# Optimization experiments

Measured on AMD Instinct MI355X. Metric: run time of the kernel, lower is better.

Reference implementation:

```python
import jax, jax.numpy as jnp
import numpy as np

N_PEP, N_MHC, N_TCR = 20000, 5000, 100000
EMB, HID = 128, 256
E_PM, E_MT = 200000, 400000
B = 50000


def setup_inputs() -> dict:
    key = jax.random.key(0)
    ks = jax.random.split(key, 30)
    f32 = jnp.float32

    def w(k, shape, fan_in):
        # torch Linear default: U(-1/sqrt(fan_in), 1/sqrt(fan_in))
        lim = 1.0 / np.sqrt(fan_in)
        return jax.random.uniform(k, shape, dtype=f32, minval=-lim, maxval=lim)

    inp = {
        # embedding tables (learned params)
        "emb_pep": jax.random.normal(ks[0], (N_PEP, EMB), dtype=f32),
        "emb_mhc": jax.random.normal(ks[1], (N_MHC, EMB), dtype=f32),
        "emb_tcr": jax.random.normal(ks[2], (N_TCR, EMB), dtype=f32),
        # edge lists (src=edge_index[0], dst=edge_index[1])
        "src_pm": jax.random.randint(ks[3], (E_PM,), 0, N_PEP, dtype=jnp.int32),
        "dst_pm": jax.random.randint(ks[4], (E_PM,), 0, N_MHC, dtype=jnp.int32),
        "src_mt": jax.random.randint(ks[5], (E_MT,), 0, N_MHC, dtype=jnp.int32),
        "dst_mt": jax.random.randint(ks[6], (E_MT,), 0, N_TCR, dtype=jnp.int32),
        # triplet pack indices
        "pack_pep": jax.random.randint(ks[7], (B,), 0, N_PEP, dtype=jnp.int32),
        "pack_mhc": jax.random.randint(ks[8], (B,), 0, N_MHC, dtype=jnp.int32),
        "pack_tcr": jax.random.randint(ks[9], (B,), 0, N_TCR, dtype=jnp.int32),
        # SAGEConv params: Wl (aggregated neighbors, with bias), Wr (root, no bias)
        # layer 1: pep->mhc (src 128, dst 128); mhc->tcr (src 128, dst 128)
        "l1_pm_Wl": w(ks[10], (HID, EMB), EMB), "l1_pm_bl": w(ks[11], (HID,), EMB),
        "l1_pm_Wr": w(ks[12], (HID, EMB), EMB),
        "l1_mt_Wl": w(ks[13], (HID, EMB), EMB), "l1_mt_bl": w(ks[14], (HID,), EMB),
        "l1_mt_Wr": w(ks[15], (HID, EMB), EMB),
        # layer 2: pep->mhc (src 128, dst 256); mhc->tcr (src 256, dst 256)
        "l2_pm_Wl": w(ks[16], (HID, EMB), EMB), "l2_pm_bl": w(ks[17], (HID,), EMB),
        "l2_pm_Wr": w(ks[18], (HID, HID), HID),
        "l2_mt_Wl": w(ks[19], (HID, HID), HID), "l2_mt_bl": w(ks[20], (HID,), HID),
        "l2_mt_Wr": w(ks[21], (HID, HID), HID),
        # proj_pep and head MLP
        "proj_W": w(ks[22], (HID, EMB), EMB), "proj_b": w(ks[23], (HID,), EMB),
        "head_W1": w(ks[24], (HID, 3 * HID), 3 * HID), "head_b1": w(ks[25], (HID,), 3 * HID),
        "head_W2": w(ks[26], (1, HID), HID), "head_b2": w(ks[27], (1,), HID),
    }
    return inp


def _sage(x_src, x_dst, src, dst, Wl, bl, Wr, n_dst):
    # SAGEConv(mean): lin_l(mean_{j in N(i)} x_src[j]) + lin_r(x_dst[i])
    msg = jax.ops.segment_sum(x_src[src], dst, num_segments=n_dst)  # [n_dst, d_src]
    cnt = jax.ops.segment_sum(jnp.ones((src.shape[0],), x_src.dtype), dst, num_segments=n_dst)
    mean = msg / jnp.maximum(cnt, 1.0)[:, None]
    return mean @ Wl.T + bl + x_dst @ Wr.T


def reference(emb_pep, emb_mhc, emb_tcr,
              src_pm, dst_pm, src_mt, dst_mt,
              pack_pep, pack_mhc, pack_tcr,
              l1_pm_Wl, l1_pm_bl, l1_pm_Wr, l1_mt_Wl, l1_mt_bl, l1_mt_Wr,
              l2_pm_Wl, l2_pm_bl, l2_pm_Wr, l2_mt_Wl, l2_mt_bl, l2_mt_Wr,
              proj_W, proj_b, head_W1, head_b1, head_W2, head_b2):
    relu = jax.nn.relu
    # layer 1 (HeteroConv reads all relations from the same input dict)
    mhc1 = relu(_sage(emb_pep, emb_mhc, src_pm, dst_pm, l1_pm_Wl, l1_pm_bl, l1_pm_Wr, N_MHC))
    tcr1 = relu(_sage(emb_mhc, emb_tcr, src_mt, dst_mt, l1_mt_Wl, l1_mt_bl, l1_mt_Wr, N_TCR))
    # layer 2 ('pep' is never a destination, so it keeps its embedding)
    mhc2 = relu(_sage(emb_pep, mhc1, src_pm, dst_pm, l2_pm_Wl, l2_pm_bl, l2_pm_Wr, N_MHC))
    tcr2 = relu(_sage(mhc1, tcr1, src_mt, dst_mt, l2_mt_Wl, l2_mt_bl, l2_mt_Wr, N_TCR))
    # projections + triplet gather (dropout disabled: inference)
    hp = (emb_pep @ proj_W.T + proj_b)[pack_pep]  # [B, HID]
    hm = mhc2[pack_mhc]
    ht = tcr2[pack_tcr]
    z = jnp.concatenate([hp, hm, ht], axis=-1)  # [B, 3*HID]
    hidden = relu(z @ head_W1.T + head_b1)
    logits = hidden @ head_W2.T + head_b2
    return logits.squeeze(-1)
```

## Files before the change

kernel.cpp:

```cpp
#include <hip/hip_runtime.h>

constexpr int NPEP = 20000, NMHC = 5000, NTCR = 100000;
constexpr int EPM = 200000, EMT = 400000, BB = 50000;
constexpr int MAXU = 50000;

typedef __attribute__((ext_vector_type(8))) short bf16x8;
typedef __attribute__((ext_vector_type(4))) float f32x4;

__device__ inline ushort f2bf(float x) {
    union { float f; unsigned u; } v; v.f = x;
    unsigned r = (v.u + 0x7FFF + ((v.u >> 16) & 1)) >> 16;
    return (ushort)r;
}
__device__ inline float bf2f(ushort b) {
    union { unsigned u; float f; } t; t.u = ((unsigned)b) << 16; return t.f;
}
__device__ inline void bf2x2(unsigned u, float& a, float& b) {
    union { unsigned x; float f; } t1, t2;
    t1.x = u << 16; t2.x = u & 0xffff0000u;
    a = t1.f; b = t2.f;
}
__device__ inline ushort4 f4bf(float4 v) {
    return make_ushort4(f2bf(v.x), f2bf(v.y), f2bf(v.z), f2bf(v.w));
}

__global__ __launch_bounds__(256) void prep_kernel(
    int* __restrict__ ibz,
    const float4* __restrict__ Wr1f, ushort4* __restrict__ Wr1_b,
    const float4* __restrict__ Wr2f, ushort4* __restrict__ Wr2_b,
    const float* __restrict__ head_W1, ushort4* __restrict__ W1b_b, ushort4* __restrict__ W1c_b,
    const float* __restrict__ l1_pm_Wl, const float* __restrict__ l1_pm_Wr,
    const float* __restrict__ l1_mt_Wl, ushort* __restrict__ Wcat1_b,
    const float* __restrict__ l2_pm_Wl, const float* __restrict__ l2_pm_Wr,
    const float* __restrict__ l2_mt_Wl, ushort* __restrict__ Wcat2_b,
    const float4* __restrict__ emb_mhc, ushort* __restrict__ Acat1,
    const float* __restrict__ proj_W, const float* __restrict__ proj_b,
    ushort* __restrict__ Wcomp_b, float* __restrict__ bp) {
    __shared__ float red[128];
    const int b = blockIdx.x, tid = threadIdx.x;
    if (b < 303) {
        int i = b * 256 + tid;
        if (i < 77500) ((int4*)ibz)[i] = make_int4(0, 0, 0, 0);
    } else if (b < 335) {
        int i = (b - 303) * 256 + tid;
        if (i < 8192) Wr1_b[i] = f4bf(Wr1f[i]);
    } else if (b < 399) {
        int i = (b - 335) * 256 + tid;
        if (i < 16384) Wr2_b[i] = f4bf(Wr2f[i]);
    } else if (b < 463) {
        int i = (b - 399) * 256 + tid;
        if (i < 16384) {
            int n = i >> 6, k4 = (i & 63) * 4;
            float4 v = *(const float4*)(head_W1 + (size_t)n * 768 + 256 + k4);
            W1b_b[i] = f4bf(v);
        }
    } else if (b < 527) {
        int i = (b - 463) * 256 + tid;
        if (i < 16384) {
            int n = i >> 6, k4 = (i & 63) * 4;
            float4 v = *(const float4*)(head_W1 + (size_t)n * 768 + 512 + k4);
            W1c_b[i] = f4bf(v);
        }
    } else if (b < 1039) {
        int idx = (b - 527) * 256 + tid;
        if (idx < 131072) {
            int r = idx >> 8, k = idx & 255;
            float v;
            if (r < 256) v = (k < 128) ? l1_pm_Wl[r * 128 + k] : l1_pm_Wr[r * 128 + (k - 128)];
            else         v = (k < 128) ? 0.f : l1_mt_Wl[(r - 256) * 128 + (k - 128)];
            Wcat1_b[idx] = f2bf(v);
        }
    } else if (b < 1807) {
        int idx = (b - 1039) * 256 + tid;
        if (idx < 196608) {
            int r = idx / 384, k = idx - r * 384;
            float v;
            if (r < 256) v = (k < 128) ? l2_pm_Wl[r * 128 + k] : l2_pm_Wr[r * 256 + (k - 128)];
            else         v = (k < 128) ? 0.f : l2_mt_Wl[(r - 256) * 256 + (k - 128)];
            Wcat2_b[idx] = f2bf(v);
        }
    } else if (b < 2432) {
        int i4 = (b - 1807) * 256 + tid;
        if (i4 < 160000) {
            int r = i4 >> 5, c4 = (i4 & 31) * 4;
            *(ushort4*)(Acat1 + (size_t)r * 256 + 128 + c4) = f4bf(emb_mhc[i4]);
        }
    } else {
        int i = b - 2432;
        const float* w1row = head_W1 + (size_t)i * 768;
        if (tid < 128) {
            float acc = 0.f;
            for (int k = 0; k < 256; k++) acc += w1row[k] * proj_W[k * 128 + tid];
            Wcomp_b[i * 128 + tid] = f2bf(acc);
            float pb = w1row[2 * tid] * proj_b[2 * tid] + w1row[2 * tid + 1] * proj_b[2 * tid + 1];
            red[tid] = pb;
        }
        __syncthreads();
        if (tid < 64) { red[tid] += red[tid + 64]; }
        __syncthreads();
        if (tid < 32) { red[tid] += red[tid + 32]; }
        __syncthreads();
        if (tid == 0) {
            float s = 0.f;
            for (int j = 0; j < 32; j++) s += red[j];
            bp[i] = s;
        }
    }
}

__global__ void hist2_kernel(const int* __restrict__ dst_pm, const int* __restrict__ dst_mt,
                             const int* __restrict__ pack_tcr,
                             int* __restrict__ deg_pm, int* __restrict__ deg_mt,
                             int* __restrict__ mark) {
    int t = blockIdx.x * blockDim.x + threadIdx.x;
    if (t < EPM) atomicAdd(&deg_pm[dst_pm[t]], 1);
    else if (t < EPM + EMT) atomicAdd(&deg_mt[dst_mt[t - EPM]], 1);
    else if (t < EPM + EMT + BB) mark[pack_tcr[t - EPM - EMT]] = 1;
}

__global__ __launch_bounds__(256) void blocksum2_kernel(const int* __restrict__ deg_pm,
                                                        const int* __restrict__ deg_mt,
                                                        const int* __restrict__ mark,
                                                        int* __restrict__ bsum_pm,
                                                        int* __restrict__ bsum_mt,
                                                        int* __restrict__ bsum_mk) {
    __shared__ int red[256];
    const int tid = threadIdx.x;
    const int* deg; int n, bi; int* bsum;
    if (blockIdx.x < 5) { deg = deg_pm; n = NMHC; bi = blockIdx.x; bsum = bsum_pm; }
    else if (blockIdx.x < 103) { deg = deg_mt; n = NTCR; bi = blockIdx.x - 5; bsum = bsum_mt; }
    else { deg = mark; n = NTCR; bi = blockIdx.x - 103; bsum = bsum_mk; }
    const int base = bi * 1024;
    int s = 0;
#pragma unroll
    for (int j = 0; j < 4; j++) {
        int i = base + tid + j * 256;
        if (i < n) s += deg[i];
    }
    red[tid] = s;
    __syncthreads();
    for (int off = 128; off > 0; off >>= 1) {
        if (tid < off) red[tid] += red[tid + off];
        __syncthreads();
    }
    if (tid == 0) bsum[bi] = red[0];
}

__global__ __launch_bounds__(128) void scanb2_kernel(int* __restrict__ bsum_pm,
                                                     int* __restrict__ bsum_mt,
                                                     int* __restrict__ bsum_mk) {
    __shared__ int s[128];
    const int tid = threadIdx.x;
    int* bsum = (blockIdx.x == 0) ? bsum_pm : ((blockIdx.x == 1) ? bsum_mt : bsum_mk);
    const int nb = (blockIdx.x == 0) ? 5 : 98;
    int v = (tid < nb) ? bsum[tid] : 0;
    s[tid] = v;
    __syncthreads();
    for (int off = 1; off < 128; off <<= 1) {
        int t = (tid >= off) ? s[tid - off] : 0;
        __syncthreads();
        s[tid] += t;
        __syncthreads();
    }
    if (tid < nb) bsum[tid] = (tid > 0) ? s[tid - 1] : 0;
    if (tid == 0) bsum[nb] = s[nb - 1];
}

__global__ __launch_bounds__(256) void emit2_kernel(const int* __restrict__ deg_pm,
                                                    const int* __restrict__ deg_mt,
                                                    const int* __restrict__ mark,
                                                    const int* __restrict__ bsum_pm,
                                                    const int* __restrict__ bsum_mt,
                                                    const int* __restrict__ bsum_mk,
                                                    int* __restrict__ rp_pm, float* __restrict__ cnt_pm,
                                                    int* __restrict__ rp_mt, float* __restrict__ cnt_mt,
                                                    int* __restrict__ list) {
    __shared__ int tsum[256];
    const int tid = threadIdx.x;
    const int* deg; const int* bsum; int* rp; float* cnt; int n, nb, bi, mode;
    if (blockIdx.x < 5) { deg = deg_pm; bsum = bsum_pm; rp = rp_pm; cnt = cnt_pm; n = NMHC; nb = 5; bi = blockIdx.x; mode = 0; }
    else if (blockIdx.x < 103) { deg = deg_mt; bsum = bsum_mt; rp = rp_mt; cnt = cnt_mt; n = NTCR; nb = 98; bi = blockIdx.x - 5; mode = 0; }
    else { deg = mark; bsum = bsum_mk; rp = nullptr; cnt = nullptr; n = NTCR; nb = 98; bi = blockIdx.x - 103; mode = 1; }
    const int i0 = bi * 1024 + tid * 4;
    int4 v = make_int4(0, 0, 0, 0);
    if (i0 + 3 < n) v = *(const int4*)(deg + i0);
    else if (i0 < n) {
        int t[4] = {0, 0, 0, 0};
        for (int j = 0; j < 4 && i0 + j < n; j++) t[j] = deg[i0 + j];
        v = make_int4(t[0], t[1], t[2], t[3]);
    }
    int s = v.x + v.y + v.z + v.w;
    tsum[tid] = s;
    __syncthreads();
    for (int off = 1; off < 256; off <<= 1) {
        int t = (tid >= off) ? tsum[tid - off] : 0;
        __syncthreads();
        tsum[tid] += t;
        __syncthreads();
    }
    int ex = ((tid > 0) ? tsum[tid - 1] : 0) + bsum[bi];
    if (mode == 0) {
        if (i0 + 3 < n) {
            int r1 = ex + v.x, r2 = r1 + v.y, r3 = r2 + v.z;
            *(int4*)(rp + i0) = make_int4(ex, r1, r2, r3);
            *(float4*)(cnt + i0) = make_float4((float)v.x, (float)v.y, (float)v.z, (float)v.w);
        } else if (i0 < n) {
            int r = ex;
            int vv[4] = {v.x, v.y, v.z, v.w};
            for (int j = 0; j < 4 && i0 + j < n; j++) {
                rp[i0 + j] = r;
                cnt[i0 + j] = (float)vv[j];
                r += vv[j];
            }
        }
        if (bi == 0 && tid == 0) rp[n] = bsum[nb];
    } else {
        int p = ex;
        int vv[4] = {v.x, v.y, v.z, v.w};
#pragma unroll
        for (int j = 0; j < 4; j++) {
            if (i0 + j < n && vv[j]) list[p++] = i0 + j;
        }
    }
}

__global__ void fill2_kernel(const int* __restrict__ src_pm, const int* __restrict__ dst_pm,
                             const int* __restrict__ src_mt, const int* __restrict__ dst_mt,
                             const int* __restrict__ rp_pm, int* __restrict__ cur_pm, int* __restrict__ csr_pm,
                             const int* __restrict__ rp_mt, int* __restrict__ cur_mt, int* __restrict__ csr_mt) {
    int t = blockIdx.x * blockDim.x + threadIdx.x;
    if (t < EPM) {
        int d = dst_pm[t];
        int pos = atomicAdd(&cur_pm[d], 1);
        csr_pm[rp_pm[d] + pos] = src_pm[t];
    } else if (t < EPM + EMT) {
        int t2 = t - EPM;
        int d = dst_mt[t2];
        int pos = atomicAdd(&cur_mt[d], 1);
        csr_mt[rp_mt[d] + pos] = src_mt[t2];
    }
}

__global__ __launch_bounds__(256) void gatherpm_kernel(const int* __restrict__ rp,
                                                       const int* __restrict__ csr_src,
                                                       const float* __restrict__ X,
                                                       ushort* __restrict__ A1, ushort* __restrict__ A2,
                                                       int n) {
    const int tid = threadIdx.x;
    const int r = blockIdx.x * 8 + (tid >> 5);
    const int lane = tid & 31;
    if (r >= n) return;
    const int e0 = rp[r], e1 = rp[r + 1];
    float4 s = make_float4(0.f, 0.f, 0.f, 0.f);
    for (int e = e0; e < e1; e++) {
        const int sidx = csr_src[e];
        float4 v = ((const float4*)(X + (long)sidx * 128))[lane];
        s.x += v.x; s.y += v.y; s.z += v.z; s.w += v.w;
    }
    float sc = 1.f / fmaxf((float)(e1 - e0), 1.f);
    ushort4 o = make_ushort4(f2bf(s.x * sc), f2bf(s.y * sc), f2bf(s.z * sc), f2bf(s.w * sc));
    *(ushort4*)(A1 + (size_t)r * 256 + lane * 4) = o;
    *(ushort4*)(A2 + (size_t)r * 384 + lane * 4) = o;
}

template <int K, int NB0, bool RELU0, bool G2>
__global__ __launch_bounds__(256, 2) void mfma_fused_kernel(
    int M, const ushort* __restrict__ A, const ushort* __restrict__ W,
    const float* __restrict__ bias,
    ushort* __restrict__ out0, int s0, ushort* __restrict__ out1) {
    constexpr int RS = 40;
    __shared__ ushort Als[128 * RS];
    __shared__ ushort Wls[128 * RS];
    const int tid = threadIdx.x;
    const int m0 = blockIdx.x * 128, n0 = blockIdx.y * 128;
    const int lane = tid & 63, w = tid >> 6;
    const int wm = w >> 1, wn = w & 1;
    const int m16 = lane & 15, q = lane >> 4;

    f32x4 acc[4][4] = {};

    for (int k0 = 0; k0 < K; k0 += 32) {
        bf16x8 a_st[2], w_st[2];
#pragma unroll
        for (int r = 0; r < 2; r++) {
            int chunk = tid + r * 256;
            int row = chunk >> 2, off = (chunk & 3) * 8;
            int ga = min(m0 + row, M - 1);
            a_st[r] = *(const bf16x8*)(A + (size_t)ga * K + k0 + off);
            w_st[r] = *(const bf16x8*)(W + (size_t)(n0 + row) * K + k0 + off);
        }
        __syncthreads();
#pragma unroll
        for (int r = 0; r < 2; r++) {
            int chunk = tid + r * 256;
            int row = chunk >> 2, off = (chunk & 3) * 8;
            *(bf16x8*)(&Als[row * RS + off]) = a_st[r];
            *(bf16x8*)(&Wls[row * RS + off]) = w_st[r];
        }
        __syncthreads();
        bf16x8 af[4], bf[4];
#pragma unroll
        for (int t = 0; t < 4; t++) {
            af[t] = *(const bf16x8*)(&Als[(wm * 64 + t * 16 + m16) * RS + q * 8]);
            bf[t] = *(const bf16x8*)(&Wls[(wn * 64 + t * 16 + m16) * RS + q * 8]);
        }
#pragma unroll
        for (int mt = 0; mt < 4; mt++)
#pragma unroll
            for (int nt = 0; nt < 4; nt++)
                acc[mt][nt] = __builtin_amdgcn_mfma_f32_16x16x32_bf16(af[mt], bf[nt], acc[mt][nt], 0, 0, 0);
    }

    const bool g1 = G2 && ((int)blockIdx.y >= NB0);
#pragma unroll
    for (int mt = 0; mt < 4; mt++) {
#pragma unroll
        for (int i = 0; i < 4; i++) {
            int row = m0 + wm * 64 + mt * 16 + q * 4 + i;
            if (row >= M) continue;
#pragma unroll
            for (int nt = 0; nt < 4; nt++) {
                int col = n0 + wn * 64 + nt * 16 + m16;
                float v = acc[mt][nt][i];
                if (!g1) {
                    v += bias[col];
                    if (RELU0) v = fmaxf(v, 0.f);
                    out0[(size_t)row * s0 + col] = f2bf(v);
                } else {
                    out1[(size_t)row * 256 + (col - NB0 * 128)] = f2bf(v);
                }
            }
        }
    }
}

__global__ __launch_bounds__(256, 3) void tcrall_kernel(
    const int* __restrict__ nrowsp, const int* __restrict__ list,
    const int* __restrict__ rp, const int* __restrict__ csr_src,
    const ushort* __restrict__ Z1, const ushort* __restrict__ Z2,
    const float* __restrict__ emb_tcr,
    const ushort* __restrict__ Wr1, const ushort* __restrict__ Wr2,
    const ushort* __restrict__ W1c,
    const float* __restrict__ bl1, const float* __restrict__ bl2,
    ushort* __restrict__ Ht) {
    constexpr int RS1 = 136;
    constexpr int RS2 = 264;
    __shared__ ushort B[32 * RS2];
    __shared__ ushort A1[32 * RS2];
    __shared__ ushort A2[32 * RS2];
    __shared__ int origs[32];
    const int tid = threadIdx.x;
    const int M = nrowsp[0];
    const int m0 = blockIdx.x * 32;
    if (m0 >= M) return;
    const int lane = tid & 63, w = tid >> 6;
    const int m16 = lane & 15, q = lane >> 4;

    if (tid < 32) origs[tid] = list[min(m0 + tid, M - 1)];

#pragma unroll
    for (int r = 0; r < 4; r++) {
        int chunk = tid + r * 256;
        int row = chunk >> 5, c4 = (chunk & 31) * 4;
        int grow = list[min(m0 + row, M - 1)];
        float4 v = *(const float4*)(emb_tcr + (size_t)grow * 128 + c4);
        *(ushort4*)(&B[row * RS1 + c4]) = f4bf(v);
    }

    {
        const int g = tid >> 5, gl = tid & 31;
        for (int rr = g; rr < 32; rr += 8) {
            int cr = min(m0 + rr, M - 1);
            int orig = list[cr];
            int e0 = rp[orig], e1 = rp[orig + 1];
            float s1[8] = {}, s2[8] = {};
            for (int e = e0; e < e1; e++) {
                int sidx = csr_src[e];
                uint4 u1 = *(const uint4*)(Z1 + (size_t)sidx * 256 + gl * 8);
                uint4 u2 = *(const uint4*)(Z2 + (size_t)sidx * 256 + gl * 8);
                float a, b;
                bf2x2(u1.x, a, b); s1[0] += a; s1[1] += b;
                bf2x2(u1.y, a, b); s1[2] += a; s1[3] += b;
                bf2x2(u1.z, a, b); s1[4] += a; s1[5] += b;
                bf2x2(u1.w, a, b); s1[6] += a; s1[7] += b;
                bf2x2(u2.x, a, b); s2[0] += a; s2[1] += b;
                bf2x2(u2.y, a, b); s2[2] += a; s2[3] += b;
                bf2x2(u2.z, a, b); s2[4] += a; s2[5] += b;
                bf2x2(u2.w, a, b); s2[6] += a; s2[7] += b;
            }
            float es = 1.f / fmaxf((float)(e1 - e0), 1.f);
            uint4 w1, w2;
            w1.x = (unsigned)f2bf(s1[0] * es) | ((unsigned)f2bf(s1[1] * es) << 16);
            w1.y = (unsigned)f2bf(s1[2] * es) | ((unsigned)f2bf(s1[3] * es) << 16);
            w1.z = (unsigned)f2bf(s1[4] * es) | ((unsigned)f2bf(s1[5] * es) << 16);
            w1.w = (unsigned)f2bf(s1[6] * es) | ((unsigned)f2bf(s1[7] * es) << 16);
            w2.x = (unsigned)f2bf(s2[0] * es) | ((unsigned)f2bf(s2[1] * es) << 16);
            w2.y = (unsigned)f2bf(s2[2] * es) | ((unsigned)f2bf(s2[3] * es) << 16);
            w2.z = (unsigned)f2bf(s2[4] * es) | ((unsigned)f2bf(s2[5] * es) << 16);
            w2.w = (unsigned)f2bf(s2[6] * es) | ((unsigned)f2bf(s2[7] * es) << 16);
            *(uint4*)(&A1[rr * RS2 + gl * 8]) = w1;
            *(uint4*)(&A2[rr * RS2 + gl * 8]) = w2;
        }
    }
    __syncthreads();

    {
        f32x4 acc[2][4] = {};
        for (int k0 = 0; k0 < 128; k0 += 32) {
            bf16x8 af[2], bf[4];
#pragma unroll
            for (int t = 0; t < 2; t++)
                af[t] = *(const bf16x8*)(&B[(t * 16 + m16) * RS1 + k0 + q * 8]);
#pragma unroll
            for (int t = 0; t < 4; t++)
                bf[t] = *(const bf16x8*)(Wr1 + (size_t)(w * 64 + t * 16 + m16) * 128 + k0 + q * 8);
#pragma unroll
            for (int mt = 0; mt < 2; mt++)
#pragma unroll
                for (int nt = 0; nt < 4; nt++)
                    acc[mt][nt] = __builtin_amdgcn_mfma_f32_16x16x32_bf16(af[mt], bf[nt], acc[mt][nt], 0, 0, 0);
        }
        __syncthreads();
#pragma unroll
        for (int mt = 0; mt < 2; mt++)
#pragma unroll
            for (int i = 0; i < 4; i++) {
                int lr = mt * 16 + q * 4 + i;
#pragma unroll
                for (int nt = 0; nt < 4; nt++) {
                    int col = w * 64 + nt * 16 + m16;
                    float v = acc[mt][nt][i] + bl1[col] + bf2f(A1[lr * RS2 + col]);
                    B[lr * RS2 + col] = f2bf(fmaxf(v, 0.f));
                }
            }
    }
    __syncthreads();

    {
        f32x4 acc[2][4] = {};
        for (int k0 = 0; k0 < 256; k0 += 32) {
            bf16x8 af[2], bf[4];
#pragma unroll
            for (int t = 0; t < 2; t++)
                af[t] = *(const bf16x8*)(&B[(t * 16 + m16) * RS2 + k0 + q * 8]);
#pragma unroll
            for (int t = 0; t < 4; t++)
                bf[t] = *(const bf16x8*)(Wr2 + (size_t)(w * 64 + t * 16 + m16) * 256 + k0 + q * 8);
#pragma unroll
            for (int mt = 0; mt < 2; mt++)
#pragma unroll
                for (int nt = 0; nt < 4; nt++)
                    acc[mt][nt] = __builtin_amdgcn_mfma_f32_16x16x32_bf16(af[mt], bf[nt], acc[mt][nt], 0, 0, 0);
        }
        __syncthreads();
#pragma unroll
        for (int mt = 0; mt < 2; mt++)
#pragma unroll
            for (int i = 0; i < 4; i++) {
                int lr = mt * 16 + q * 4 + i;
#pragma unroll
                for (int nt = 0; nt < 4; nt++) {
                    int col = w * 64 + nt * 16 + m16;
                    float v = acc[mt][nt][i] + bl2[col] + bf2f(A2[lr * RS2 + col]);
                    B[lr * RS2 + col] = f2bf(fmaxf(v, 0.f));
                }
            }
    }
    __syncthreads();

    {
        f32x4 acc[2][4] = {};
        for (int k0 = 0; k0 < 256; k0 += 32) {
            bf16x8 af[2], bf[4];
#pragma unroll
            for (int t = 0; t < 2; t++)
                af[t] = *(const bf16x8*)(&B[(t * 16 + m16) * RS2 + k0 + q * 8]);
#pragma unroll
            for (int t = 0; t < 4; t++)
                bf[t] = *(const bf16x8*)(W1c + (size_t)(w * 64 + t * 16 + m16) * 256 + k0 + q * 8);
#pragma unroll
            for (int mt = 0; mt < 2; mt++)
#pragma unroll
                for (int nt = 0; nt < 4; nt++)
                    acc[mt][nt] = __builtin_amdgcn_mfma_f32_16x16x32_bf16(af[mt], bf[nt], acc[mt][nt], 0, 0, 0);
        }
        __syncthreads();
#pragma unroll
        for (int mt = 0; mt < 2; mt++)
#pragma unroll
            for (int i = 0; i < 4; i++) {
                int lr = mt * 16 + q * 4 + i;
#pragma unroll
                for (int nt = 0; nt < 4; nt++) {
                    int col = w * 64 + nt * 16 + m16;
                    B[lr * RS2 + col] = f2bf(acc[mt][nt][i]);
                }
            }
    }
    __syncthreads();

#pragma unroll
    for (int r = 0; r < 4; r++) {
        int chunk = tid + r * 256;
        int row = chunk >> 5, c8 = (chunk & 31) * 8;
        if (m0 + row < M)
            *(uint4*)(Ht + (size_t)origs[row] * 256 + c8) = *(const uint4*)(&B[row * RS2 + c8]);
    }
}

template <int K, bool HASB, bool AF32>
__global__ __launch_bounds__(256, 2) void mfma_out_kernel(
    int M, const void* __restrict__ Av, const ushort* __restrict__ W,
    const float* __restrict__ bias, ushort* __restrict__ out) {
    constexpr int RS = 40;
    __shared__ ushort Als[128 * RS];
    __shared__ ushort Wls[128 * RS];
    const int tid = threadIdx.x;
    const int m0 = blockIdx.x * 128, n0 = blockIdx.y * 128;
    const int lane = tid & 63, w = tid >> 6;
    const int wm = w >> 1, wn = w & 1;
    const int m16 = lane & 15, q = lane >> 4;

    f32x4 acc[4][4] = {};

    for (int k0 = 0; k0 < K; k0 += 32) {
        bf16x8 a_st[2], w_st[2];
#pragma unroll
        for (int r = 0; r < 2; r++) {
            int chunk = tid + r * 256;
            int row = chunk >> 2, off = (chunk & 3) * 8;
            int ga = min(m0 + row, M - 1);
            if constexpr (AF32) {
                const float* Af = (const float*)Av;
                float4 f0 = *(const float4*)(Af + (size_t)ga * K + k0 + off);
                float4 f1 = *(const float4*)(Af + (size_t)ga * K + k0 + off + 4);
                ushort4 u0 = f4bf(f0), u1 = f4bf(f1);
                bf16x8 av;
                av[0] = (short)u0.x; av[1] = (short)u0.y; av[2] = (short)u0.z; av[3] = (short)u0.w;
                av[4] = (short)u1.x; av[5] = (short)u1.y; av[6] = (short)u1.z; av[7] = (short)u1.w;
                a_st[r] = av;
            } else {
                a_st[r] = *(const bf16x8*)((const ushort*)Av + (size_t)ga * K + k0 + off);
            }
            w_st[r] = *(const bf16x8*)(W + (size_t)(n0 + row) * K + k0 + off);
        }
        __syncthreads();
#pragma unroll
        for (int r = 0; r < 2; r++) {
            int chunk = tid + r * 256;
            int row = chunk >> 2, off = (chunk & 3) * 8;
            *(bf16x8*)(&Als[row * RS + off]) = a_st[r];
            *(bf16x8*)(&Wls[row * RS + off]) = w_st[r];
        }
        __syncthreads();
        bf16x8 af[4], bf[4];
#pragma unroll
        for (int t = 0; t < 4; t++) {
            af[t] = *(const bf16x8*)(&Als[(wm * 64 + t * 16 + m16) * RS + q * 8]);
            bf[t] = *(const bf16x8*)(&Wls[(wn * 64 + t * 16 + m16) * RS + q * 8]);
        }
#pragma unroll
        for (int mt = 0; mt < 4; mt++)
#pragma unroll
            for (int nt = 0; nt < 4; nt++)
                acc[mt][nt] = __builtin_amdgcn_mfma_f32_16x16x32_bf16(af[mt], bf[nt], acc[mt][nt], 0, 0, 0);
    }

#pragma unroll
    for (int mt = 0; mt < 4; mt++) {
#pragma unroll
        for (int i = 0; i < 4; i++) {
            int row = m0 + wm * 64 + mt * 16 + q * 4 + i;
            if (row >= M) continue;
#pragma unroll
            for (int nt = 0; nt < 4; nt++) {
                int col = n0 + wn * 64 + nt * 16 + m16;
                float v = acc[mt][nt][i];
                if (HASB) v += bias[col];
                out[(size_t)row * 256 + col] = f2bf(v);
            }
        }
    }
}

__global__ __launch_bounds__(256) void combine_kernel(
    const ushort* __restrict__ Hp, const ushort* __restrict__ Hm, const ushort* __restrict__ Ht,
    const int* __restrict__ pp, const int* __restrict__ pm, const int* __restrict__ pt,
    const float* __restrict__ b1, const float* __restrict__ W2, const float* __restrict__ b2,
    float* __restrict__ out) {
    const int tid = threadIdx.x;
    const int lane = tid & 63, w = tid >> 6;
    const int c = lane * 4;
    const float4 b1v = *(const float4*)(b1 + c);
    const float4 w2v = *(const float4*)(W2 + c);
    const float b2v = b2[0];
    const int base = blockIdx.x * 32 + w * 8;
#pragma unroll
    for (int t = 0; t < 8; t++) {
        int i = base + t;
        if (i >= BB) return;
        int ra = pp[i], rb = pm[i], rc = pt[i];
        ushort4 ua = *(const ushort4*)(Hp + (size_t)ra * 256 + c);
        ushort4 ub = *(const ushort4*)(Hm + (size_t)rb * 256 + c);
        ushort4 uc = *(const ushort4*)(Ht + (size_t)rc * 256 + c);
        float h0 = fmaxf(bf2f(ua.x) + bf2f(ub.x) + bf2f(uc.x) + b1v.x, 0.f);
        float h1 = fmaxf(bf2f(ua.y) + bf2f(ub.y) + bf2f(uc.y) + b1v.y, 0.f);
        float h2 = fmaxf(bf2f(ua.z) + bf2f(ub.z) + bf2f(uc.z) + b1v.z, 0.f);
        float h3 = fmaxf(bf2f(ua.w) + bf2f(ub.w) + bf2f(uc.w) + b1v.w, 0.f);
        float p = h0 * w2v.x + h1 * w2v.y + h2 * w2v.z + h3 * w2v.w;
#pragma unroll
        for (int off = 32; off > 0; off >>= 1) p += __shfl_down(p, off);
        if (lane == 0) out[i] = p + b2v;
    }
}

extern "C" void kernel_launch(void* const* d_in, const int* in_sizes, int n_in,
                              void* d_out, int out_size, void* d_ws, size_t ws_size,
                              hipStream_t stream) {
    const float* emb_pep = (const float*)d_in[0];
    const float* emb_mhc = (const float*)d_in[1];
    const float* emb_tcr = (const float*)d_in[2];
    const int* src_pm = (const int*)d_in[3];
    const int* dst_pm = (const int*)d_in[4];
    const int* src_mt = (const int*)d_in[5];
    const int* dst_mt = (const int*)d_in[6];
    const int* pack_pep = (const int*)d_in[7];
    const int* pack_mhc = (const int*)d_in[8];
    const int* pack_tcr = (const int*)d_in[9];
    const float* l1_pm_Wl = (const float*)d_in[10];
    const float* l1_pm_bl = (const float*)d_in[11];
    const float* l1_pm_Wr = (const float*)d_in[12];
    const float* l1_mt_Wl = (const float*)d_in[13];
    const float* l1_mt_bl = (const float*)d_in[14];
    const float* l1_mt_Wr = (const float*)d_in[15];
    const float* l2_pm_Wl = (const float*)d_in[16];
    const float* l2_pm_bl = (const float*)d_in[17];
    const float* l2_pm_Wr = (const float*)d_in[18];
    const float* l2_mt_Wl = (const float*)d_in[19];
    const float* l2_mt_bl = (const float*)d_in[20];
    const float* l2_mt_Wr = (const float*)d_in[21];
    const float* proj_W = (const float*)d_in[22];
    const float* proj_b = (const float*)d_in[23];
    const float* head_W1 = (const float*)d_in[24];
    const float* head_b1 = (const float*)d_in[25];
    const float* head_W2 = (const float*)d_in[26];
    const float* head_b2 = (const float*)d_in[27];
    float* out = (float*)d_out;

    int* ib = (int*)d_ws;
    int* deg_pm = ib;
    int* cur_pm = ib + 5000;
    int* deg_mt = ib + 10000;
    int* cur_mt = ib + 110000;
    int* mark   = ib + 210000;
    int* rp_pm  = ib + 310000;
    int* rp_mt  = ib + 315008;
    int* csr_pm = ib + 415016;
    int* csr_mt = ib + 615016;
    int* bsum_pm = ib + 1015016;
    int* bsum_mt = ib + 1015176;
    int* bsum_mk = ib + 1015336;
    int* list    = ib + 1015496;

    float* f = (float*)(ib + 1065544);
    float* cnt_pm = f;
    float* cnt_mt = f + 5000;
    float* bp     = f + 105000;

    ushort* u = (ushort*)(f + 105344);
    ushort* Wcat1_b = u;
    ushort* Wcat2_b = u + 131072;
    ushort* W1b_b   = u + 327680;
    ushort* W1c_b   = u + 393216;
    ushort* Wcomp_b = u + 458752;
    ushort* Wr1_b   = u + 491520;
    ushort* Wr2_b   = u + 524288;
    ushort* Acat1   = u + 589824;
    ushort* Acat2   = u + 1869824;
    ushort* Zb1     = u + 3789824;
    ushort* Zb2     = u + 5069824;
    ushort* mhc2_b  = u + 6349824;
    ushort* Hp_b    = u + 7629824;
    ushort* Hm_b    = u + 12749824;
    ushort* Ht_b    = u + 14029824;

    prep_kernel<<<2688, 256, 0, stream>>>(
        ib,
        (const float4*)l1_mt_Wr, (ushort4*)Wr1_b,
        (const float4*)l2_mt_Wr, (ushort4*)Wr2_b,
        head_W1, (ushort4*)W1b_b, (ushort4*)W1c_b,
        l1_pm_Wl, l1_pm_Wr, l1_mt_Wl, Wcat1_b,
        l2_pm_Wl, l2_pm_Wr, l2_mt_Wl, Wcat2_b,
        (const float4*)emb_mhc, Acat1,
        proj_W, proj_b, Wcomp_b, bp);

    hist2_kernel<<<(EPM + EMT + BB + 255) / 256, 256, 0, stream>>>(
        dst_pm, dst_mt, pack_tcr, deg_pm, deg_mt, mark);
    blocksum2_kernel<<<201, 256, 0, stream>>>(deg_pm, deg_mt, mark, bsum_pm, bsum_mt, bsum_mk);
    scanb2_kernel<<<3, 128, 0, stream>>>(bsum_pm, bsum_mt, bsum_mk);
    emit2_kernel<<<201, 256, 0, stream>>>(deg_pm, deg_mt, mark, bsum_pm, bsum_mt, bsum_mk,
                                          rp_pm, cnt_pm, rp_mt, cnt_mt, list);
    fill2_kernel<<<(EPM + EMT + 255) / 256, 256, 0, stream>>>(
        src_pm, dst_pm, src_mt, dst_mt, rp_pm, cur_pm, csr_pm, rp_mt, cur_mt, csr_mt);

    gatherpm_kernel<<<(NMHC + 7) / 8, 256, 0, stream>>>(rp_pm, csr_pm, emb_pep, Acat1, Acat2, NMHC);

    mfma_fused_kernel<256, 2, true, true><<<dim3((NMHC + 127) / 128, 4), 256, 0, stream>>>(
        NMHC, Acat1, Wcat1_b, l1_pm_bl, Acat2 + 128, 384, Zb1);
    mfma_fused_kernel<384, 2, true, true><<<dim3((NMHC + 127) / 128, 4), 256, 0, stream>>>(
        NMHC, Acat2, Wcat2_b, l2_pm_bl, mhc2_b, 256, Zb2);

    tcrall_kernel<<<(MAXU + 31) / 32, 256, 0, stream>>>(
        bsum_mk + 98, list, rp_mt, csr_mt, Zb1, Zb2, emb_tcr,
        Wr1_b, Wr2_b, W1c_b, l1_mt_bl, l2_mt_bl, Ht_b);

    mfma_out_kernel<128, true, true><<<dim3((NPEP + 127) / 128, 2), 256, 0, stream>>>(
        NPEP, emb_pep, Wcomp_b, bp, Hp_b);
    mfma_out_kernel<256, false, false><<<dim3((NMHC + 127) / 128, 2), 256, 0, stream>>>(
        NMHC, mhc2_b, W1b_b, nullptr, Hm_b);

    combine_kernel<<<(BB + 31) / 32, 256, 0, stream>>>(
        Hp_b, Hm_b, Ht_b, pack_pep, pack_mhc, pack_tcr,
        head_b1, head_W2, head_b2, out);
}
```

Measured before the change: 416.3 us.

## Merge output GEMMs into gather/tcr kernels and compact TCR output rows

Folds the two standalone output GEMM launches into existing kernels by block-range dispatch: the pep projection tile runs inside the MHC gather kernel, and the mhc2×W1b tile runs inside the TCR kernel using a shared-memory union. The TCR kernel now writes results to compacted rows, with an inverse map built during emit and a remapped pack_tcr index used by combine, so the scattered stores to a full 100k-row buffer go away. The neighbor loop preloads up to 32 CSR indices per lane and broadcasts them with shuffles, and the unused float degree-count writes are removed. This cuts launch count and scattered traffic, but adds an extra indirection buffer and gives the merged kernels uneven per-block work.

```diff
diff --git a/kernel.cpp b/kernel.cpp
--- a/kernel.cpp
+++ b/kernel.cpp
@@ -22,6 +22,81 @@
 }
 __device__ inline ushort4 f4bf(float4 v) {
     return make_ushort4(f2bf(v.x), f2bf(v.y), f2bf(v.z), f2bf(v.w));
+}
+
+constexpr int RS  = 40;
+constexpr int RS1 = 136;
+constexpr int RS2 = 264;
+
+template <int K, bool HASB, bool AF32>
+__device__ void out_tile(ushort* Als, ushort* Wls, int tid, int bx, int by, int M,
+                         const void* __restrict__ Av, const ushort* __restrict__ W,
+                         const float* __restrict__ bias, ushort* __restrict__ out) {
+    const int m0 = bx * 128, n0 = by * 128;
+    const int lane = tid & 63, w = tid >> 6;
+    const int wm = w >> 1, wn = w & 1;
+    const int m16 = lane & 15, q = lane >> 4;
+
+    f32x4 acc[4][4] = {};
+
+    for (int k0 = 0; k0 < K; k0 += 32) {
+        bf16x8 a_st[2], w_st[2];
+#pragma unroll
+        for (int r = 0; r < 2; r++) {
+            int chunk = tid + r * 256;
+            int row = chunk >> 2, off = (chunk & 3) * 8;
+            int ga = min(m0 + row, M - 1);
+            if constexpr (AF32) {
+                const float* Af = (const float*)Av;
+                float4 f0 = *(const float4*)(Af + (size_t)ga * K + k0 + off);
+                float4 f1 = *(const float4*)(Af + (size_t)ga * K + k0 + off + 4);
+                ushort4 u0 = f4bf(f0), u1 = f4bf(f1);
+                bf16x8 av;
+                av[0] = (short)u0.x; av[1] = (short)u0.y; av[2] = (short)u0.z; av[3] = (short)u0.w;
+                av[4] = (short)u1.x; av[5] = (short)u1.y; av[6] = (short)u1.z; av[7] = (short)u1.w;
+                a_st[r] = av;
+            } else {
+                a_st[r] = *(const bf16x8*)((const ushort*)Av + (size_t)ga * K + k0 + off);
+            }
+            w_st[r] = *(const bf16x8*)(W + (size_t)(n0 + row) * K + k0 + off);
+        }
+        __syncthreads();
+#pragma unroll
+        for (int r = 0; r < 2; r++) {
+            int chunk = tid + r * 256;
+            int row = chunk >> 2, off = (chunk & 3) * 8;
+            *(bf16x8*)(&Als[row * RS + off]) = a_st[r];
+            *(bf16x8*)(&Wls[row * RS + off]) = w_st[r];
+        }
+        __syncthreads();
+        bf16x8 af[4], bf[4];
+#pragma unroll
+        for (int t = 0; t < 4; t++) {
+            af[t] = *(const bf16x8*)(&Als[(wm * 64 + t * 16 + m16) * RS + q * 8]);
+            bf[t] = *(const bf16x8*)(&Wls[(wn * 64 + t * 16 + m16) * RS + q * 8]);
+        }
+#pragma unroll
+        for (int mt = 0; mt < 4; mt++)
+#pragma unroll
+            for (int nt = 0; nt < 4; nt++)
+                acc[mt][nt] = __builtin_amdgcn_mfma_f32_16x16x32_bf16(af[mt], bf[nt], acc[mt][nt], 0, 0, 0);
+    }
+
+#pragma unroll
+    for (int mt = 0; mt < 4; mt++) {
+#pragma unroll
+        for (int i = 0; i < 4; i++) {
+            int row = m0 + wm * 64 + mt * 16 + q * 4 + i;
+            if (row >= M) continue;
+#pragma unroll
+            for (int nt = 0; nt < 4; nt++) {
+                int col = n0 + wn * 64 + nt * 16 + m16;
+                float v = acc[mt][nt][i];
+                if (HASB) v += bias[col];
+                out[(size_t)row * 256 + col] = f2bf(v);
+            }
+        }
+    }
 }
 
 __global__ __launch_bounds__(256) void prep_kernel(
@@ -51,15 +126,13 @@
         int i = (b - 399) * 256 + tid;
         if (i < 16384) {
             int n = i >> 6, k4 = (i & 63) * 4;
-            float4 v = *(const float4*)(head_W1 + (size_t)n * 768 + 256 + k4);
-            W1b_b[i] = f4bf(v);
+            W1b_b[i] = f4bf(*(const float4*)(head_W1 + (size_t)n * 768 + 256 + k4));
         }
     } else if (b < 527) {
         int i = (b - 463) * 256 + tid;
         if (i < 16384) {
             int n = i >> 6, k4 = (i & 63) * 4;
-            float4 v = *(const float4*)(head_W1 + (size_t)n * 768 + 512 + k4);
-            W1c_b[i] = f4bf(v);
+            W1c_b[i] = f4bf(*(const float4*)(head_W1 + (size_t)n * 768 + 512 + k4));
         }
     } else if (b < 1039) {
         int idx = (b - 527) * 256 + tid;
@@ -92,8 +165,7 @@
             float acc = 0.f;
             for (int k = 0; k < 256; k++) acc += w1row[k] * proj_W[k * 128 + tid];
             Wcomp_b[i * 128 + tid] = f2bf(acc);
-            float pb = w1row[2 * tid] * proj_b[2 * tid] + w1row[2 * tid + 1] * proj_b[2 * tid + 1];
-            red[tid] = pb;
+            red[tid] = w1row[2 * tid] * proj_b[2 * tid] + w1row[2 * tid + 1] * proj_b[2 * tid + 1];
         }
         __syncthreads();
         if (tid < 64) { red[tid] += red[tid + 64]; }
@@ -172,15 +244,16 @@
                                                     const int* __restrict__ bsum_pm,
                                                     const int* __restrict__ bsum_mt,
                                                     const int* __restrict__ bsum_mk,
-                                                    int* __restrict__ rp_pm, float* __restrict__ cnt_pm,
-                                                    int* __restrict__ rp_mt, float* __restrict__ cnt_mt,
-                                                    int* __restrict__ list) {
+                                                    int* __restrict__ rp_pm,
+                                                    int* __restrict__ rp_mt,
+                                                    int* __restrict__ list,
+                                                    int* __restrict__ inv) {
     __shared__ int tsum[256];
     const int tid = threadIdx.x;
-    const int* deg; const int* bsum; int* rp; float* cnt; int n, nb, bi, mode;
-    if (blockIdx.x < 5) { deg = deg_pm; bsum = bsum_pm; rp = rp_pm; cnt = cnt_pm; n = NMHC; nb = 5; bi = blockIdx.x; mode = 0; }
-    else if (blockIdx.x < 103) { deg = deg_mt; bsum = bsum_mt; rp = rp_mt; cnt = cnt_mt; n = NTCR; nb = 98; bi = blockIdx.x - 5; mode = 0; }
-    else { deg = mark; bsum = bsum_mk; rp = nullptr; cnt = nullptr; n = NTCR; nb = 98; bi = blockIdx.x - 103; mode = 1; }
+    const int* deg; const int* bsum; int* rp; int n, nb, bi, mode;
+    if (blockIdx.x < 5) { deg = deg_pm; bsum = bsum_pm; rp = rp_pm; n = NMHC; nb = 5; bi = blockIdx.x; mode = 0; }
+    else if (blockIdx.x < 103) { deg = deg_mt; bsum = bsum_mt; rp = rp_mt; n = NTCR; nb = 98; bi = blockIdx.x - 5; mode = 0; }
+    else { deg = mark; bsum = bsum_mk; rp = nullptr; n = NTCR; nb = 98; bi = blockIdx.x - 103; mode = 1; }
     const int i0 = bi * 1024 + tid * 4;
     int4 v = make_int4(0, 0, 0, 0);
     if (i0 + 3 < n) v = *(const int4*)(deg + i0);
@@ -189,8 +262,7 @@
         for (int j = 0; j < 4 && i0 + j < n; j++) t[j] = deg[i0 + j];
         v = make_int4(t[0], t[1], t[2], t[3]);
     }
-    int s = v.x + v.y + v.z + v.w;
-    tsum[tid] = s;
+    tsum[tid] = v.x + v.y + v.z + v.w;
     __syncthreads();
     for (int off = 1; off < 256; off <<= 1) {
         int t = (tid >= off) ? tsum[tid - off] : 0;
@@ -203,15 +275,10 @@
         if (i0 + 3 < n) {
             int r1 = ex + v.x, r2 = r1 + v.y, r3 = r2 + v.z;
             *(int4*)(rp + i0) = make_int4(ex, r1, r2, r3);
-            *(float4*)(cnt + i0) = make_float4((float)v.x, (float)v.y, (float)v.z, (float)v.w);
         } else if (i0 < n) {
             int r = ex;
             int vv[4] = {v.x, v.y, v.z, v.w};
-            for (int j = 0; j < 4 && i0 + j < n; j++) {
-                rp[i0 + j] = r;
-                cnt[i0 + j] = (float)vv[j];
-                r += vv[j];
-            }
+            for (int j = 0; j < 4 && i0 + j < n; j++) { rp[i0 + j] = r; r += vv[j]; }
         }
         if (bi == 0 && tid == 0) rp[n] = bsum[nb];
     } else {
@@ -219,7 +286,7 @@
         int vv[4] = {v.x, v.y, v.z, v.w};
 #pragma unroll
         for (int j = 0; j < 4; j++) {
-            if (i0 + j < n && vv[j]) list[p++] = i0 + j;
+            if (i0 + j < n && vv[j]) { list[p] = i0 + j; inv[i0 + j] = p; p++; }
         }
     }
 }
@@ -241,26 +308,39 @@
     }
 }
 
-__global__ __launch_bounds__(256) void gatherpm_kernel(const int* __restrict__ rp,
-                                                       const int* __restrict__ csr_src,
-                                                       const float* __restrict__ X,
-                                                       ushort* __restrict__ A1, ushort* __restrict__ A2,
-                                                       int n) {
+__global__ __launch_bounds__(256, 2) void gph_kernel(
+    const int* __restrict__ rp, const int* __restrict__ csr_src,
+    const float* __restrict__ X, ushort* __restrict__ A1, ushort* __restrict__ A2,
+    const float* __restrict__ emb_pep, const ushort* __restrict__ Wcomp,
+    const float* __restrict__ bp, ushort* __restrict__ Hp,
+    const int* __restrict__ pack_tcr, const int* __restrict__ inv, int* __restrict__ pt_c) {
+    __shared__ ushort Als[128 * RS];
+    __shared__ ushort Wls[128 * RS];
     const int tid = threadIdx.x;
-    const int r = blockIdx.x * 8 + (tid >> 5);
-    const int lane = tid & 31;
-    if (r >= n) return;
-    const int e0 = rp[r], e1 = rp[r + 1];
-    float4 s = make_float4(0.f, 0.f, 0.f, 0.f);
-    for (int e = e0; e < e1; e++) {
-        const int sidx = csr_src[e];
-        float4 v = ((const float4*)(X + (long)sidx * 128))[lane];
-        s.x += v.x; s.y += v.y; s.z += v.z; s.w += v.w;
-    }
-    float sc = 1.f / fmaxf((float)(e1 - e0), 1.f);
-    ushort4 o = make_ushort4(f2bf(s.x * sc), f2bf(s.y * sc), f2bf(s.z * sc), f2bf(s.w * sc));
-    *(ushort4*)(A1 + (size_t)r * 256 + lane * 4) = o;
-    *(ushort4*)(A2 + (size_t)r * 384 + lane * 4) = o;
+    const int b = blockIdx.x;
+    if (b < 625) {
+        const int r = b * 8 + (tid >> 5);
+        const int lane = tid & 31;
+        if (r >= NMHC) return;
+        const int e0 = rp[r], e1 = rp[r + 1];
+        float4 s = make_float4(0.f, 0.f, 0.f, 0.f);
+        for (int e = e0; e < e1; e++) {
+            const int sidx = csr_src[e];
+            float4 v = ((const float4*)(X + (long)sidx * 128))[lane];
+            s.x += v.x; s.y += v.y; s.z += v.z; s.w += v.w;
+        }
+        float sc = 1.f / fmaxf((float)(e1 - e0), 1.f);
+        ushort4 o = make_ushort4(f2bf(s.x * sc), f2bf(s.y * sc), f2bf(s.z * sc), f2bf(s.w * sc));
+        *(ushort4*)(A1 + (size_t)r * 256 + lane * 4) = o;
+        *(ushort4*)(A2 + (size_t)r * 384 + lane * 4) = o;
+    } else if (b < 939) {
+        int v = b - 625;
+        out_tile<128, true, true>(Als, Wls, tid, v % 157, v / 157, NPEP,
+                                  emb_pep, Wcomp, bp, Hp);
+    } else {
+        int i = (b - 939) * 256 + tid;
+        if (i < BB) pt_c[i] = inv[pack_tcr[i]];
+    }
 }
 
 template <int K, int NB0, bool RELU0, bool G2>
@@ -268,7 +348,6 @@
     int M, const ushort* __restrict__ A, const ushort* __restrict__ W,
     const float* __restrict__ bias,
     ushort* __restrict__ out0, int s0, ushort* __restrict__ out1) {
-    constexpr int RS = 40;
     __shared__ ushort Als[128 * RS];
     __shared__ ushort Wls[128 * RS];
     const int tid = threadIdx.x;
@@ -334,7 +413,7 @@
     }
 }
 
-__global__ __launch_bounds__(256, 3) void tcrall_kernel(
+__global__ __launch_bounds__(256, 3) void tcrhm_kernel(
     const int* __restrict__ nrowsp, const int* __restrict__ list,
     const int* __restrict__ rp, const int* __restrict__ csr_src,
     const ushort* __restrict__ Z1, const ushort* __restrict__ Z2,
@@ -342,29 +421,36 @@
     const ushort* __restrict__ Wr1, const ushort* __restrict__ Wr2,
     const ushort* __restrict__ W1c,
     const float* __restrict__ bl1, const float* __restrict__ bl2,
-    ushort* __restrict__ Ht) {
-    constexpr int RS1 = 136;
-    constexpr int RS2 = 264;
-    __shared__ ushort B[32 * RS2];
-    __shared__ ushort A1[32 * RS2];
-    __shared__ ushort A2[32 * RS2];
-    __shared__ int origs[32];
+    ushort* __restrict__ Ht_c,
+    const ushort* __restrict__ mhc2, const ushort* __restrict__ W1b,
+    ushort* __restrict__ Hm) {
+    union SM {
+        struct { ushort B[32 * RS2]; ushort A1[32 * RS2]; ushort A2[32 * RS2]; } t;
+        struct { ushort Als[128 * RS]; ushort Wls[128 * RS]; } g;
+    };
+    __shared__ SM sm;
     const int tid = threadIdx.x;
+
+    if (blockIdx.x >= 1563) {
+        int v = blockIdx.x - 1563;
+        out_tile<256, false, false>(sm.g.Als, sm.g.Wls, tid, v % 40, v / 40, NMHC,
+                                    mhc2, W1b, nullptr, Hm);
+        return;
+    }
+
     const int M = nrowsp[0];
     const int m0 = blockIdx.x * 32;
     if (m0 >= M) return;
     const int lane = tid & 63, w = tid >> 6;
     const int m16 = lane & 15, q = lane >> 4;
 
-    if (tid < 32) origs[tid] = list[min(m0 + tid, M - 1)];
-
 #pragma unroll
     for (int r = 0; r < 4; r++) {
         int chunk = tid + r * 256;
         int row = chunk >> 5, c4 = (chunk & 31) * 4;
         int grow = list[min(m0 + row, M - 1)];
         float4 v = *(const float4*)(emb_tcr + (size_t)grow * 128 + c4);
-        *(ushort4*)(&B[row * RS1 + c4]) = f4bf(v);
+        *(ushort4*)(&sm.t.B[row * RS1 + c4]) = f4bf(v);
     }
 
     {
@@ -373,22 +459,39 @@
             int cr = min(m0 + rr, M - 1);
             int orig = list[cr];
             int e0 = rp[orig], e1 = rp[orig + 1];
+            int deg = e1 - e0;
             float s1[8] = {}, s2[8] = {};
-            for (int e = e0; e < e1; e++) {
+            int sidx_l = (gl < deg) ? csr_src[e0 + gl] : 0;
+            int dn = min(deg, 32);
+            for (int e = 0; e < dn; e++) {
+                int sidx = __shfl(sidx_l, e, 32);
+                uint4 u1 = *(const uint4*)(Z1 + (size_t)sidx * 256 + gl * 8);
+                uint4 u2 = *(const uint4*)(Z2 + (size_t)sidx * 256 + gl * 8);
+                float x, y;
+                bf2x2(u1.x, x, y); s1[0] += x; s1[1] += y;
+                bf2x2(u1.y, x, y); s1[2] += x; s1[3] += y;
+                bf2x2(u1.z, x, y); s1[4] += x; s1[5] += y;
+                bf2x2(u1.w, x, y); s1[6] += x; s1[7] += y;
+                bf2x2(u2.x, x, y); s2[0] += x; s2[1] += y;
+                bf2x2(u2.y, x, y); s2[2] += x; s2[3] += y;
+                bf2x2(u2.z, x, y); s2[4] += x; s2[5] += y;
+                bf2x2(u2.w, x, y); s2[6] += x; s2[7] += y;
+            }
+            for (int e = e0 + 32; e < e1; e++) {
                 int sidx = csr_src[e];
                 uint4 u1 = *(const uint4*)(Z1 + (size_t)sidx * 256 + gl * 8);
                 uint4 u2 = *(const uint4*)(Z2 + (size_t)sidx * 256 + gl * 8);
-                float a, b;
-                bf2x2(u1.x, a, b); s1[0] += a; s1[1] += b;
-                bf2x2(u1.y, a, b); s1[2] += a; s1[3] += b;
-                bf2x2(u1.z, a, b); s1[4] += a; s1[5] += b;
-                bf2x2(u1.w, a, b); s1[6] += a; s1[7] += b;
-                bf2x2(u2.x, a, b); s2[0] += a; s2[1] += b;
-                bf2x2(u2.y, a, b); s2[2] += a; s2[3] += b;
-                bf2x2(u2.z, a, b); s2[4] += a; s2[5] += b;
-                bf2x2(u2.w, a, b); s2[6] += a; s2[7] += b;
+                float x, y;
+                bf2x2(u1.x, x, y); s1[0] += x; s1[1] += y;
+                bf2x2(u1.y, x, y); s1[2] += x; s1[3] += y;
+                bf2x2(u1.z, x, y); s1[4] += x; s1[5] += y;
+                bf2x2(u1.w, x, y); s1[6] += x; s1[7] += y;
+                bf2x2(u2.x, x, y); s2[0] += x; s2[1] += y;
+                bf2x2(u2.y, x, y); s2[2] += x; s2[3] += y;
+                bf2x2(u2.z, x, y); s2[4] += x; s2[5] += y;
+                bf2x2(u2.w, x, y); s2[6] += x; s2[7] += y;
             }
-            float es = 1.f / fmaxf((float)(e1 - e0), 1.f);
+            float es = 1.f / fmaxf((float)deg, 1.f);
             uint4 w1, w2;
             w1.x = (unsigned)f2bf(s1[0] * es) | ((unsigned)f2bf(s1[1] * es) << 16);
             w1.y = (unsigned)f2bf(s1[2] * es) | ((unsigned)f2bf(s1[3] * es) << 16);
@@ -398,8 +501,8 @@
             w2.y = (unsigned)f2bf(s2[2] * es) | ((unsigned)f2bf(s2[3] * es) << 16);
             w2.z = (unsigned)f2bf(s2[4] * es) | ((unsigned)f2bf(s2[5] * es) << 16);
             w2.w = (unsigned)f2bf(s2[6] * es) | ((unsigned)f2bf(s2[7] * es) << 16);
-            *(uint4*)(&A1[rr * RS2 + gl * 8]) = w1;
-            *(uint4*)(&A2[rr * RS2 + gl * 8]) = w2;
+            *(uint4*)(&sm.t.A1[rr * RS2 + gl * 8]) = w1;
+            *(uint4*)(&sm.t.A2[rr * RS2 + gl * 8]) = w2;
         }
     }
     __syncthreads();
@@ -410,7 +513,7 @@
             bf16x8 af[2], bf[4];
 #pragma unroll
             for (int t = 0; t < 2; t++)
-                af[t] = *(const bf16x8*)(&B[(t * 16 + m16) * RS1 + k0 + q * 8]);
+                af[t] = *(const bf16x8*)(&sm.t.B[(t * 16 + m16) * RS1 + k0 + q * 8]);
 #pragma unroll
             for (int t = 0; t < 4; t++)
                 bf[t] = *(const bf16x8*)(Wr1 + (size_t)(w * 64 + t * 16 + m16) * 128 + k0 + q * 8);
@@ -429,8 +532,8 @@
 #pragma unroll
                 for (int nt = 0; nt < 4; nt++) {
                     int col = w * 64 + nt * 16 + m16;
-                    float v = acc[mt][nt][i] + bl1[col] + bf2f(A1[lr * RS2 + col]);
-                    B[lr * RS2 + col] = f2bf(fmaxf(v, 0.f));
+                    float v = acc[mt][nt][i] + bl1[col] + bf2f(sm.t.A1[lr * RS2 + col]);
+                    sm.t.B[lr * RS2 + col] = f2bf(fmaxf(v, 0.f));
                 }
             }
     }
@@ -442,7 +545,7 @@
             bf16x8 af[2], bf[4];
 #pragma unroll
             for (int t = 0; t < 2; t++)
-                af[t] = *(const bf16x8*)(&B[(t * 16 + m16) * RS2 + k0 + q * 8]);
+                af[t] = *(const bf16x8*)(&sm.t.B[(t * 16 + m16) * RS2 + k0 + q * 8]);
 #pragma unroll
             for (int t = 0; t < 4; t++)
                 bf[t] = *(const bf16x8*)(Wr2 + (size_t)(w * 64 + t * 16 + m16) * 256 + k0 + q * 8);
@@ -461,8 +564,8 @@
 #pragma unroll
                 for (int nt = 0; nt < 4; nt++) {
                     int col = w * 64 + nt * 16 + m16;
-                    float v = acc[mt][nt][i] + bl2[col] + bf2f(A2[lr * RS2 + col]);
-                    B[lr * RS2 + col] = f2bf(fmaxf(v, 0.f));
+                    float v = acc[mt][nt][i] + bl2[col] + bf2f(sm.t.A2[lr * RS2 + col]);
+                    sm.t.B[lr * RS2 + col] = f2bf(fmaxf(v, 0.f));
                 }
             }
     }
@@ -474,7 +577,7 @@
             bf16x8 af[2], bf[4];
 #pragma unroll
             for (int t = 0; t < 2; t++)
-                af[t] = *(const bf16x8*)(&B[(t * 16 + m16) * RS2 + k0 + q * 8]);
+                af[t] = *(const bf16x8*)(&sm.t.B[(t * 16 + m16) * RS2 + k0 + q * 8]);
 #pragma unroll
             for (int t = 0; t < 4; t++)
                 bf[t] = *(const bf16x8*)(W1c + (size_t)(w * 64 + t * 16 + m16) * 256 + k0 + q * 8);
@@ -493,7 +596,7 @@
 #pragma unroll
                 for (int nt = 0; nt < 4; nt++) {
                     int col = w * 64 + nt * 16 + m16;
-                    B[lr * RS2 + col] = f2bf(acc[mt][nt][i]);
+                    sm.t.B[lr * RS2 + col] = f2bf(acc[mt][nt][i]);
                 }
             }
     }
@@ -504,88 +607,13 @@
         int chunk = tid + r * 256;
         int row = chunk >> 5, c8 = (chunk & 31) * 8;
         if (m0 + row < M)
-            *(uint4*)(Ht + (size_t)origs[row] * 256 + c8) = *(const uint4*)(&B[row * RS2 + c8]);
-    }
-}
-
-template <int K, bool HASB, bool AF32>
-__global__ __launch_bounds__(256, 2) void mfma_out_kernel(
-    int M, const void* __restrict__ Av, const ushort* __restrict__ W,
-    const float* __restrict__ bias, ushort* __restrict__ out) {
-    constexpr int RS = 40;
-    __shared__ ushort Als[128 * RS];
-    __shared__ ushort Wls[128 * RS];
-    const int tid = threadIdx.x;
-    const int m0 = blockIdx.x * 128, n0 = blockIdx.y * 128;
-    const int lane = tid & 63, w = tid >> 6;
-    const int wm = w >> 1, wn = w & 1;
-    const int m16 = lane & 15, q = lane >> 4;
-
-    f32x4 acc[4][4] = {};
-
-    for (int k0 = 0; k0 < K; k0 += 32) {
-        bf16x8 a_st[2], w_st[2];
-#pragma unroll
-        for (int r = 0; r < 2; r++) {
-            int chunk = tid + r * 256;
-            int row = chunk >> 2, off = (chunk & 3) * 8;
-            int ga = min(m0 + row, M - 1);
-            if constexpr (AF32) {
-                const float* Af = (const float*)Av;
-                float4 f0 = *(const float4*)(Af + (size_t)ga * K + k0 + off);
-                float4 f1 = *(const float4*)(Af + (size_t)ga * K + k0 + off + 4);
-                ushort4 u0 = f4bf(f0), u1 = f4bf(f1);
-                bf16x8 av;
-                av[0] = (short)u0.x; av[1] = (short)u0.y; av[2] = (short)u0.z; av[3] = (short)u0.w;
-                av[4] = (short)u1.x; av[5] = (short)u1.y; av[6] = (short)u1.z; av[7] = (short)u1.w;
-                a_st[r] = av;
-            } else {
-                a_st[r] = *(const bf16x8*)((const ushort*)Av + (size_t)ga * K + k0 + off);
-            }
-            w_st[r] = *(const bf16x8*)(W + (size_t)(n0 + row) * K + k0 + off);
-        }
-        __syncthreads();
-#pragma unroll
-        for (int r = 0; r < 2; r++) {
-            int chunk = tid + r * 256;
-            int row = chunk >> 2, off = (chunk & 3) * 8;
-            *(bf16x8*)(&Als[row * RS + off]) = a_st[r];
-            *(bf16x8*)(&Wls[row * RS + off]) = w_st[r];
-        }
-        __syncthreads();
-        bf16x8 af[4], bf[4];
-#pragma unroll
-        for (int t = 0; t < 4; t++) {
-            af[t] = *(const bf16x8*)(&Als[(wm * 64 + t * 16 + m16) * RS + q * 8]);
-            bf[t] = *(const bf16x8*)(&Wls[(wn * 64 + t * 16 + m16) * RS + q * 8]);
-        }
-#pragma unroll
-        for (int mt = 0; mt < 4; mt++)
-#pragma unroll
-            for (int nt = 0; nt < 4; nt++)
-                acc[mt][nt] = __builtin_amdgcn_mfma_f32_16x16x32_bf16(af[mt], bf[nt], acc[mt][nt], 0, 0, 0);
-    }
-
-#pragma unroll
-    for (int mt = 0; mt < 4; mt++) {
-#pragma unroll
-        for (int i = 0; i < 4; i++) {
-            int row = m0 + wm * 64 + mt * 16 + q * 4 + i;
-            if (row >= M) continue;
-#pragma unroll
-            for (int nt = 0; nt < 4; nt++) {
-                int col = n0 + wn * 64 + nt * 16 + m16;
-                float v = acc[mt][nt][i];
-                if (HASB) v += bias[col];
-                out[(size_t)row * 256 + col] = f2bf(v);
-            }
-        }
+            *(uint4*)(Ht_c + (size_t)(m0 + row) * 256 + c8) = *(const uint4*)(&sm.t.B[row * RS2 + c8]);
     }
 }
 
 __global__ __launch_bounds__(256) void combine_kernel(
     const ushort* __restrict__ Hp, const ushort* __restrict__ Hm, const ushort* __restrict__ Ht,
-    const int* __restrict__ pp, const int* __restrict__ pm, const int* __restrict__ pt,
+    const int* __restrict__ pp, const int* __restrict__ pm, const int* __restrict__ pt_c,
     const float* __restrict__ b1, const float* __restrict__ W2, const float* __restrict__ b2,
     float* __restrict__ out) {
     const int tid = threadIdx.x;
@@ -599,7 +627,7 @@
     for (int t = 0; t < 8; t++) {
         int i = base + t;
         if (i >= BB) return;
-        int ra = pp[i], rb = pm[i], rc = pt[i];
+        int ra = pp[i], rb = pm[i], rc = pt_c[i];
         ushort4 ua = *(const ushort4*)(Hp + (size_t)ra * 256 + c);
         ushort4 ub = *(const ushort4*)(Hm + (size_t)rb * 256 + c);
         ushort4 uc = *(const ushort4*)(Ht + (size_t)rc * 256 + c);
@@ -661,13 +689,13 @@
     int* bsum_mt = ib + 1015176;
     int* bsum_mk = ib + 1015336;
     int* list    = ib + 1015496;
-
-    float* f = (float*)(ib + 1065544);
-    float* cnt_pm = f;
-    float* cnt_mt = f + 5000;
-    float* bp     = f + 105000;
-
-    ushort* u = (ushort*)(f + 105344);
+    int* inv     = ib + 1065544;
+    int* pt_c    = ib + 1165544;
+
+    float* f = (float*)(ib + 1215592);
+    float* bp = f;
+
+    ushort* u = (ushort*)(f + 256);
     ushort* Wcat1_b = u;
     ushort* Wcat2_b = u + 131072;
     ushort* W1b_b   = u + 327680;
@@ -682,7 +710,7 @@
     ushort* mhc2_b  = u + 6349824;
     ushort* Hp_b    = u + 7629824;
     ushort* Hm_b    = u + 12749824;
-    ushort* Ht_b    = u + 14029824;
+    ushort* Ht_c    = u + 14029824;
 
     prep_kernel<<<2688, 256, 0, stream>>>(
         ib,
@@ -699,27 +727,26 @@
     blocksum2_kernel<<<201, 256, 0, stream>>>(deg_pm, deg_mt, mark, bsum_pm, bsum_mt, bsum_mk);
     scanb2_kernel<<<3, 128, 0, stream>>>(bsum_pm, bsum_mt, bsum_mk);
     emit2_kernel<<<201, 256, 0, stream>>>(deg_pm, deg_mt, mark, bsum_pm, bsum_mt, bsum_mk,
-                                          rp_pm, cnt_pm, rp_mt, cnt_mt, list);
+                                          rp_pm, rp_mt, list, inv);
     fill2_kernel<<<(EPM + EMT + 255) / 256, 256, 0, stream>>>(
         src_pm, dst_pm, src_mt, dst_mt, rp_pm, cur_pm, csr_pm, rp_mt, cur_mt, csr_mt);
 
-    gatherpm_kernel<<<(NMHC + 7) / 8, 256, 0, stream>>>(rp_pm, csr_pm, emb_pep, Acat1, Acat2, NMHC);
+    gph_kernel<<<1135, 256, 0, stream>>>(
+        rp_pm, csr_pm, emb_pep, Acat1, Acat2,
+        emb_pep, Wcomp_b, bp, Hp_b,
+        pack_tcr, inv, pt_c);
 
     mfma_fused_kernel<256, 2, true, true><<<dim3((NMHC + 127) / 128, 4), 256, 0, stream>>>(
         NMHC, Acat1, Wcat1_b, l1_pm_bl, Acat2 + 128, 384, Zb1);
     mfma_fused_kernel<384, 2, true, true><<<dim3((NMHC + 127) / 128, 4), 256, 0, stream>>>(
         NMHC, Acat2, Wcat2_b, l2_pm_bl, mhc2_b, 256, Zb2);
 
-    tcrall_kernel<<<(MAXU + 31) / 32, 256, 0, stream>>>(
+    tcrhm_kernel<<<1563 + 80, 256, 0, stream>>>(
         bsum_mk + 98, list, rp_mt, csr_mt, Zb1, Zb2, emb_tcr,
-        Wr1_b, Wr2_b, W1c_b, l1_mt_bl, l2_mt_bl, Ht_b);
-
-    mfma_out_kernel<128, true, true><<<dim3((NPEP + 127) / 128, 2), 256, 0, stream>>>(
-        NPEP, emb_pep, Wcomp_b, bp, Hp_b);
-    mfma_out_kernel<256, false, false><<<dim3((NMHC + 127) / 128, 2), 256, 0, stream>>>(
-        NMHC, mhc2_b, W1b_b, nullptr, Hm_b);
+        Wr1_b, Wr2_b, W1c_b, l1_mt_bl, l2_mt_bl, Ht_c,
+        mhc2_b, W1b_b, Hm_b);
 
     combine_kernel<<<(BB + 31) / 32, 256, 0, stream>>>(
-        Hp_b, Hm_b, Ht_b, pack_pep, pack_mhc, pack_tcr,
+        Hp_b, Hm_b, Ht_c, pack_pep, pack_mhc, pt_c,
         head_b1, head_W2, head_b2, out);
 }
```

Result: faster. 385.1 us (-7.5%).
